# Optimization experiments

Measured on AMD Instinct MI355X. Metric: run time of the kernel, lower is better.

Reference implementation:

```python
import jax, jax.numpy as jnp
import numpy as np

B, S, D, H, F, V, T, L = 64, 1024, 256, 256, 128, 50000, 64, 8
H2 = 2 * H
DIN = H2 + D + 3 * F  # 1152


def setup_inputs() -> dict:
    key = jax.random.key(0)
    ks = jax.random.split(key, 12)
    sd = 0.05
    return {
        "word_ids": jax.random.randint(ks[0], (B, S), 1, V, dtype=jnp.int32),
        "embed": jax.random.normal(ks[1], (V, D), jnp.float32) * sd,
        "encoder_outputs": jax.random.normal(ks[2], (B, S, H2), jnp.float32) * sd,
        "wconv1": jax.random.normal(ks[3], (F, 1, D), jnp.float32) * sd,
        "bconv1": jax.random.normal(ks[4], (F,), jnp.float32) * sd,
        "wconv2": jax.random.normal(ks[5], (F, 2, D), jnp.float32) * sd,
        "bconv2": jax.random.normal(ks[6], (F,), jnp.float32) * sd,
        "wconv3": jax.random.normal(ks[7], (F, 3, D), jnp.float32) * sd,
        "bconv3": jax.random.normal(ks[8], (F,), jnp.float32) * sd,
        "W_ih": jax.random.normal(ks[9], (4 * H2, DIN), jnp.float32) * sd,
        "W_hh": jax.random.normal(ks[10], (4 * H2, H2), jnp.float32) * sd,
        "W_fc": jax.random.normal(ks[11], (T, H2), jnp.float32) * sd,
        "seg_len": L,
    }


def reference(word_ids, embed, encoder_outputs, wconv1, bconv1, wconv2, bconv2,
              wconv3, bconv3, W_ih, W_hh, W_fc, seg_len):
    b, s = word_ids.shape
    d = embed.shape[1]
    h2 = encoder_outputs.shape[-1]
    h = h2 // 2
    nseg = s // seg_len

    # word features via embedding lookup (WordFeature with single 'word' feature)
    wf = embed[word_ids]                                  # [B, S, D]
    xs = wf.reshape(b, nseg, seg_len, d)                  # [B, nseg, L, D]
    c_w = xs.mean(axis=2)                                 # [B, nseg, D]
    es = encoder_outputs.reshape(b, nseg, seg_len, h2)
    c_h = es.mean(axis=2)                                 # [B, nseg, 2H]

    # char-CNN per segment: conv2d(1->F, (fs, D)) == 1D conv over time with D in-channels
    xc = xs.reshape(b * nseg, seg_len, d).transpose(0, 2, 1)  # [N, D, L]

    def conv_pool(w, bias):
        k = w.transpose(0, 2, 1)                          # [F, D, fs]
        y = jax.lax.conv_general_dilated(xc, k, window_strides=(1,),
                                         padding="VALID",
                                         dimension_numbers=("NCH", "OIH", "NCH"))
        y = jax.nn.relu(y + bias[None, :, None])
        return y.max(axis=2)                              # max-pool over time -> [N, F]

    c_x = jnp.concatenate([conv_pool(wconv1, bconv1),
                           conv_pool(wconv2, bconv2),
                           conv_pool(wconv3, bconv3)], axis=1)
    c_x = c_x.reshape(b, nseg, -1)                        # [B, nseg, 3F]

    dec_in = jnp.concatenate([c_w, c_h, c_x], axis=-1)    # [B, nseg, DIN]

    # decoder init: fwd-last / bwd-first encoder states
    h0 = jnp.concatenate([encoder_outputs[:, -1, :h], encoder_outputs[:, 0, h:]], axis=1)
    c0 = jnp.zeros_like(h0)

    def step(carry, x):
        hh, cc = carry
        gates = x @ W_ih.T + hh @ W_hh.T                  # [B, 4*2H]
        i, fg, g, o = jnp.split(gates, 4, axis=1)
        cc = jax.nn.sigmoid(fg) * cc + jax.nn.sigmoid(i) * jnp.tanh(g)
        hh = jax.nn.sigmoid(o) * jnp.tanh(cc)
        out = jax.nn.log_softmax(hh @ W_fc.T, axis=-1)
        return (hh, cc), out

    _, outs = jax.lax.scan(step, (h0, c0), dec_in.transpose(1, 0, 2))  # [nseg, B, T]
    return outs.transpose(1, 0, 2).reshape(b * nseg, -1)  # batch-major like the torch loop
```

## Files before the change

kernel.cpp:

```cpp
#include <hip/hip_runtime.h>
#include <math.h>

#define BB   64
#define SS   1024
#define DD   256
#define H2   512
#define FF   128
#define TT   64
#define NSEG 128
#define DIN  1152
#define G4   2048
#define MROWS 8192
#define MX   65536

typedef __attribute__((ext_vector_type(8))) short bf16x8;
typedef __attribute__((ext_vector_type(4))) float f32x4;

__device__ __forceinline__ unsigned short f2b(float f){
    union { float f; unsigned u; } v; v.f = f;
    unsigned r = v.u + 0x7fffu + ((v.u >> 16) & 1u);
    return (unsigned short)(r >> 16);
}
__device__ __forceinline__ float b2f(unsigned short h){
    union { unsigned u; float f; } v; v.u = ((unsigned)h) << 16;
    return v.f;
}
__device__ __forceinline__ float fsig(float x){
    return 1.f / (1.f + __expf(-x));
}
__device__ __forceinline__ float ftanh(float x){
    float e = __expf(-2.f * fabsf(x));
    float r = (1.f - e) / (1.f + e);
    return x < 0.f ? -r : r;
}


__global__ void k_cvt(const float* __restrict__ src, unsigned short* __restrict__ dst, int n){
    int i = blockIdx.x * 256 + threadIdx.x;
    if (i < n) dst[i] = f2b(src[i]);
}

__global__ void k_wf(const float* __restrict__ w1, const float* __restrict__ w2,
                     const float* __restrict__ w3, unsigned short* __restrict__ Wf){
    int i = blockIdx.x * 256 + threadIdx.x;
    int col = i >> 8, d = i & 255;
    float v;
    if (col < 128)      v = w1[col * 256 + d];
    else if (col < 384) { int f = (col - 128) & 127; int tap = (col - 128) >> 7; v = w2[f * 512 + tap * 256 + d]; }
    else                { int c = col - 384; int f = c & 127; int tap = c >> 7;  v = w3[f * 768 + tap * 256 + d]; }
    Wf[i] = f2b(v);
}

__global__ void k_tr_wfc(const float* __restrict__ src, float* __restrict__ dst){
    int i = blockIdx.x * 256 + threadIdx.x;
    int v = i >> 9, k = i & 511;
    dst[k * 64 + v] = src[i];
}

__global__ void k_gather(const int* __restrict__ wid, const float* __restrict__ embed,
                         unsigned short* __restrict__ X){
    int i = blockIdx.x * 256 + threadIdx.x;
    int row = i >> 6, d4 = i & 63;
    int w = wid[row];
    float4 v = *(const float4*)(embed + (size_t)w * DD + d4 * 4);
    ushort4 o; o.x = f2b(v.x); o.y = f2b(v.y); o.z = f2b(v.z); o.w = f2b(v.w);
    *(ushort4*)(X + (size_t)row * DD + d4 * 4) = o;
}

__global__ void k_cw(const unsigned short* __restrict__ X, unsigned short* __restrict__ dec){
    int i = blockIdx.x * 256 + threadIdx.x;
    int row = i >> 8, d = i & 255;
    const unsigned short* p = X + (size_t)row * 8 * DD + d;
    float s = 0.f;
#pragma unroll
    for (int t = 0; t < 8; t++) s += b2f(p[t * DD]);
    dec[(size_t)row * DIN + d] = f2b(s * 0.125f);
}

__global__ void k_ch(const float* __restrict__ enc, unsigned short* __restrict__ dec){
    int i = blockIdx.x * 256 + threadIdx.x;
    int row = i >> 9, c = i & 511;
    const float* p = enc + (size_t)row * 8 * H2 + c;
    float s = 0.f;
#pragma unroll
    for (int t = 0; t < 8; t++) s += p[t * H2];
    dec[(size_t)row * DIN + 256 + c] = f2b(s * 0.125f);
}

__global__ void k_h0(const float* __restrict__ enc, unsigned short* __restrict__ Hbuf){
    int i = blockIdx.x * 256 + threadIdx.x;
    int b = i >> 9, c = i & 511;
    float v = (c < 256) ? enc[(size_t)b * SS * H2 + (size_t)(SS - 1) * H2 + c]
                        : enc[(size_t)b * SS * H2 + c];
    v = fminf(fmaxf(v, -1.875f), 1.875f);
    Hbuf[(size_t)b * 512 + c] = f2b(v);
}

__global__ void k_fill(uint4* __restrict__ p){
    int i = blockIdx.x * 256 + threadIdx.x;
    uint4 v; v.x = v.y = v.z = v.w = 0x7FC07FC0u;
    p[i] = v;
}

__global__ __launch_bounds__(256) void gemm_bt(
    const unsigned short* __restrict__ A, const unsigned short* __restrict__ Bm,
    unsigned short* __restrict__ C, int M, int N, int K)
{
    __shared__ unsigned short As[128][40];
    __shared__ unsigned short Bs[128][40];
    const int tid = threadIdx.x;
    const int m0 = blockIdx.y * 128, n0 = blockIdx.x * 128;
    const int w = tid >> 6, lane = tid & 63;
    const int lm = lane & 15, quad = lane >> 4;
    const int wm = (w >> 1) * 64, wn = (w & 1) * 64;

    const f32x4 z = {0.f, 0.f, 0.f, 0.f};
    f32x4 acc[4][4];
#pragma unroll
    for (int i = 0; i < 4; i++)
#pragma unroll
        for (int j = 0; j < 4; j++) acc[i][j] = z;

    const int r0 = tid >> 2;
    const int kp = (tid & 3) * 8;

    for (int kc = 0; kc < K; kc += 32){
        uint4 a0 = *(const uint4*)(A + (size_t)(m0 + r0) * K + kc + kp);
        uint4 a1 = *(const uint4*)(A + (size_t)(m0 + 64 + r0) * K + kc + kp);
        uint4 b0 = *(const uint4*)(Bm + (size_t)(n0 + r0) * K + kc + kp);
        uint4 b1 = *(const uint4*)(Bm + (size_t)(n0 + 64 + r0) * K + kc + kp);
        __syncthreads();
        *(uint4*)&As[r0][kp] = a0;
        *(uint4*)&As[64 + r0][kp] = a1;
        *(uint4*)&Bs[r0][kp] = b0;
        *(uint4*)&Bs[64 + r0][kp] = b1;
        __syncthreads();
        bf16x8 af[4], bf[4];
#pragma unroll
        for (int mt = 0; mt < 4; mt++) af[mt] = *(const bf16x8*)&As[wm + mt * 16 + lm][quad * 8];
#pragma unroll
        for (int nt = 0; nt < 4; nt++) bf[nt] = *(const bf16x8*)&Bs[wn + nt * 16 + lm][quad * 8];
#pragma unroll
        for (int mt = 0; mt < 4; mt++)
#pragma unroll
            for (int nt = 0; nt < 4; nt++)
                acc[mt][nt] = __builtin_amdgcn_mfma_f32_16x16x32_bf16(af[mt], bf[nt], acc[mt][nt], 0, 0, 0);
    }
#pragma unroll
    for (int mt = 0; mt < 4; mt++){
        int mrow = m0 + wm + mt * 16 + quad * 4;
#pragma unroll
        for (int nt = 0; nt < 4; nt++){
            int ncol = n0 + wn + nt * 16 + lm;
#pragma unroll
            for (int r = 0; r < 4; r++)
                C[(size_t)(mrow + r) * N + ncol] = f2b(acc[mt][nt][r]);
        }
    }
}

__global__ __launch_bounds__(256) void gemm_bt_gates(
    const unsigned short* __restrict__ A, const unsigned short* __restrict__ Bm,
    unsigned short* __restrict__ C, int M, int N, int K)
{
    __shared__ unsigned short As[128][40];
    __shared__ unsigned short Bs[128][40];
    const int tid = threadIdx.x;
    const int m0 = blockIdx.y * 128, n0 = blockIdx.x * 128;
    const int w = tid >> 6, lane = tid & 63;
    const int lm = lane & 15, quad = lane >> 4;
    const int wm = (w >> 1) * 64, wn = (w & 1) * 64;

    const f32x4 z = {0.f, 0.f, 0.f, 0.f};
    f32x4 acc[4][4];
#pragma unroll
    for (int i = 0; i < 4; i++)
#pragma unroll
        for (int j = 0; j < 4; j++) acc[i][j] = z;

    const int r0 = tid >> 2;
    const int kp = (tid & 3) * 8;

    for (int kc = 0; kc < K; kc += 32){
        uint4 a0 = *(const uint4*)(A + (size_t)(m0 + r0) * K + kc + kp);
        uint4 a1 = *(const uint4*)(A + (size_t)(m0 + 64 + r0) * K + kc + kp);
        uint4 b0 = *(const uint4*)(Bm + (size_t)(n0 + r0) * K + kc + kp);
        uint4 b1 = *(const uint4*)(Bm + (size_t)(n0 + 64 + r0) * K + kc + kp);
        __syncthreads();
        *(uint4*)&As[r0][kp] = a0;
        *(uint4*)&As[64 + r0][kp] = a1;
        *(uint4*)&Bs[r0][kp] = b0;
        *(uint4*)&Bs[64 + r0][kp] = b1;
        __syncthreads();
        bf16x8 af[4], bf[4];
#pragma unroll
        for (int mt = 0; mt < 4; mt++) af[mt] = *(const bf16x8*)&As[wm + mt * 16 + lm][quad * 8];
#pragma unroll
        for (int nt = 0; nt < 4; nt++) bf[nt] = *(const bf16x8*)&Bs[wn + nt * 16 + lm][quad * 8];
#pragma unroll
        for (int mt = 0; mt < 4; mt++)
#pragma unroll
            for (int nt = 0; nt < 4; nt++)
                acc[mt][nt] = __builtin_amdgcn_mfma_f32_16x16x32_bf16(af[mt], bf[nt], acc[mt][nt], 0, 0, 0);
    }
#pragma unroll
    for (int mt = 0; mt < 4; mt++){
        int mrow = m0 + wm + mt * 16 + quad * 4;
#pragma unroll
        for (int nt = 0; nt < 4; nt++){
            int ncol = n0 + wn + nt * 16 + lm;
            int g = ncol >> 9, c = ncol & 511;
            int gb = c >> 5, hcl = c & 31;
            int n = hcl * 4 + g;
#pragma unroll
            for (int r = 0; r < 4; r++){
                int m = mrow + r;
                int b = m >> 7, t = m & 127;
                int grp = b >> 4, bl = b & 15;
                size_t dst = (((size_t)(grp * 16 + gb) * NSEG + t) * 128 + n) * 16 + bl;
                C[dst] = f2b(acc[mt][nt][r]);
            }
        }
    }
}

__global__ void k_pool(const unsigned short* __restrict__ G, const float* __restrict__ bias,
                       unsigned short* __restrict__ dec, int taps, int colofs){
    int i = blockIdx.x * 256 + threadIdx.x;
    int row = i >> 7, f = i & 127;
    int N = taps * 128;
    float mx = -1e30f;
    for (int t = 0; t <= 8 - taps; t++){
        float a = 0.f;
        for (int tap = 0; tap < taps; tap++)
            a += b2f(G[(size_t)(row * 8 + t + tap) * N + tap * 128 + f]);
        mx = fmaxf(mx, a);
    }
    mx = fmaxf(mx + bias[f], 0.f);
    dec[(size_t)row * DIN + 768 + colofs + f] = f2b(mx);
}

__global__ __launch_bounds__(256, 1) void k_lstm(
    const unsigned short* __restrict__ gxt,
    const unsigned short* __restrict__ Whh,
    unsigned short* __restrict__ Hbuf)
{
    __shared__ unsigned short W_lds[128 * 512];
    __shared__ unsigned short h_lds[16 * 512];
    __shared__ unsigned short hpk[4 * 128];

    const int tid = threadIdx.x;
    const int nb = blockIdx.x;
    const int grp = nb >> 4, gb = nb & 15;
    const int w = tid >> 6, lane = tid & 63, lm = lane & 15, quad = lane >> 4;
    const int g = lm & 3;

#pragma unroll
    for (int i = 0; i < 32; i++){
        int c = i * 256 + tid;
        int n = c >> 6, kc = c & 63;
        int grow = (n & 3) * 512 + gb * 32 + (n >> 2);
        uint4 v = *(const uint4*)(Whh + (size_t)grow * H2 + kc * 8);
        unsigned addr = ((unsigned)n << 10) + ((unsigned)kc << 4);
        addr ^= (unsigned)(n & 7) << 4;
        *(uint4*)((char*)W_lds + addr) = v;
    }
    __syncthreads();

    const char* wb = (const char*)W_lds;
    const unsigned r0b = (unsigned)(w * 32 + lm) << 10;
    const unsigned r1b = r0b + (16u << 10);
    const unsigned swz = (unsigned)(lm & 7) << 4;

    float cst[2][4] = {{0.f,0.f,0.f,0.f},{0.f,0.f,0.f,0.f}};

    union Chunk { unsigned long long q[2]; uint4 u4; };

    for (int t = 0; t < NSEG; t++){
        const unsigned short* hsrc = Hbuf + (size_t)t * (BB * H2) + (size_t)grp * (16 * H2);
        Chunk ch[4];
#pragma unroll
        for (int j = 0; j < 4; j++){
            const unsigned long long* p = (const unsigned long long*)(hsrc + (size_t)(j * 256 + tid) * 8);
            ch[j].q[0] = __hip_atomic_load(p,     __ATOMIC_RELAXED, __HIP_MEMORY_SCOPE_AGENT);
            ch[j].q[1] = __hip_atomic_load(p + 1, __ATOMIC_RELAXED, __HIP_MEMORY_SCOPE_AGENT);
        }

        const unsigned short* gchunk = gxt + ((size_t)nb * NSEG + t) * 2048;
        ushort4 pr0 = *(const ushort4*)(gchunk + (w * 32 + lm) * 16 + quad * 4);
        ushort4 pr1 = *(const ushort4*)(gchunk + (w * 32 + 16 + lm) * 16 + quad * 4);

        unsigned pend = 0xFu;
        while (pend){
            unsigned np = 0;
#pragma unroll
            for (int j = 0; j < 4; j++){
                if (pend & (1u << j)){
                    if (((ch[j].q[0] | ch[j].q[1]) & 0x4000400040004000ULL) != 0ULL){
                        const unsigned long long* p = (const unsigned long long*)(hsrc + (size_t)(j * 256 + tid) * 8);
                        ch[j].q[0] = __hip_atomic_load(p,     __ATOMIC_RELAXED, __HIP_MEMORY_SCOPE_AGENT);
                        ch[j].q[1] = __hip_atomic_load(p + 1, __ATOMIC_RELAXED, __HIP_MEMORY_SCOPE_AGENT);
                        np |= 1u << j;
                    }
                }
            }
            pend = np;
            if (pend) __builtin_amdgcn_s_sleep(1);
        }

        char* hb = (char*)h_lds;
#pragma unroll
        for (int j = 0; j < 4; j++){
            unsigned addr = (unsigned)(j * 256 + tid) * 16u;
            addr ^= ((addr >> 10) & 7u) << 4;
            *(uint4*)(hb + addr) = ch[j].u4;
        }
        __syncthreads();

        const unsigned hrowb = (unsigned)lm << 10;
        f32x4 acc0 = {0.f,0.f,0.f,0.f}, acc1 = {0.f,0.f,0.f,0.f};
#pragma unroll
        for (int ks = 0; ks < 16; ks++){
            unsigned colb = ((unsigned)ks << 6) + ((unsigned)quad << 4);
            bf16x8 avv = *(const bf16x8*)(hb + ((hrowb + colb) ^ swz));
            bf16x8 w0  = *(const bf16x8*)(wb + ((r0b  + colb) ^ swz));
            bf16x8 w1  = *(const bf16x8*)(wb + ((r1b  + colb) ^ swz));
            acc0 = __builtin_amdgcn_mfma_f32_16x16x32_bf16(avv, w0, acc0, 0, 0, 0);
            acc1 = __builtin_amdgcn_mfma_f32_16x16x32_bf16(avv, w1, acc1, 0, 0, 0);
        }
        __syncthreads();

        const unsigned short* pr0s = (const unsigned short*)&pr0;
        const unsigned short* pr1s = (const unsigned short*)&pr1;
#pragma unroll
        for (int nt = 0; nt < 2; nt++){
#pragma unroll
            for (int r = 0; r < 4; r++){
                float a = (nt ? acc1[r] : acc0[r]) + b2f(nt ? pr1s[r] : pr0s[r]);
                float bsw = __shfl_xor(a, 1);
                float p  = (g & 1) ? bsw : a;
                float qq = (g & 1) ? a : bsw;
                float c2 = __shfl_xor(p, 2);
                float d2 = __shfl_xor(qq, 2);
                float iv = (g & 2) ? c2 : p;
                float gv = (g & 2) ? p  : c2;
                float fv = (g & 2) ? d2 : qq;
                float ov = (g & 2) ? qq : d2;
                float si = fsig(iv), sf = fsig(fv), so = fsig(ov);
                float cn = sf * cst[nt][r] + si * ftanh(gv);
                cst[nt][r] = cn;
                unsigned short hv = f2b(so * ftanh(cn));
                if (hv & 0x4000u) hv = 0;
                if (g == 0)
                    hpk[w * 128 + (quad * 4 + r) * 8 + nt * 4 + (lm >> 2)] = hv;
            }
        }
        asm volatile("s_waitcnt lgkmcnt(0)" ::: "memory");
        __builtin_amdgcn_sched_barrier(0);
        if (lane < 16){
            const unsigned long long* sp = (const unsigned long long*)&hpk[w * 128 + lane * 8];
            unsigned long long s0 = sp[0], s1 = sp[1];
            unsigned long long* dp = (unsigned long long*)
                (Hbuf + (size_t)(t + 1) * (BB * H2) + (size_t)(grp * 16 + lane) * H2 + gb * 32 + w * 8);
            __hip_atomic_store(dp,     s0, __ATOMIC_RELAXED, __HIP_MEMORY_SCOPE_AGENT);
            __hip_atomic_store(dp + 1, s1, __ATOMIC_RELAXED, __HIP_MEMORY_SCOPE_AGENT);
        }
        asm volatile("" ::: "memory");
    }
}

__global__ __launch_bounds__(256) void k_out(
    const unsigned short* __restrict__ Hbuf, const float* __restrict__ Wt, float* __restrict__ out)
{
    __shared__ float hsh[4][H2];
    const int w = threadIdx.x >> 6, lane = threadIdx.x & 63;
    const int row = blockIdx.x * 4 + w;
    const int b = row >> 7, t = row & 127;
    const unsigned short* hp = Hbuf + (size_t)(t + 1) * (BB * H2) + (size_t)b * H2;
    uint4 hv = *(const uint4*)(hp + lane * 8);
    const unsigned short* hs = (const unsigned short*)&hv;
#pragma unroll
    for (int i = 0; i < 8; i++) hsh[w][lane * 8 + i] = b2f(hs[i]);
    __syncthreads();
    float acc = 0.f;
#pragma unroll 8
    for (int k = 0; k < H2; k++)
        acc = fmaf(hsh[w][k], Wt[k * 64 + lane], acc);
    float m = acc;
#pragma unroll
    for (int off = 32; off; off >>= 1) m = fmaxf(m, __shfl_xor(m, off));
    float e = expf(acc - m), s = e;
#pragma unroll
    for (int off = 32; off; off >>= 1) s += __shfl_xor(s, off);
    out[(size_t)row * TT + lane] = acc - m - logf(s);
}

extern "C" void kernel_launch(void* const* d_in, const int* in_sizes, int n_in,
                              void* d_out, int out_size, void* d_ws, size_t ws_size,
                              hipStream_t stream)
{
    const int*   wid = (const int*)d_in[0];
    const float* emb = (const float*)d_in[1];
    const float* enc = (const float*)d_in[2];
    const float* wc1 = (const float*)d_in[3];
    const float* bc1 = (const float*)d_in[4];
    const float* wc2 = (const float*)d_in[5];
    const float* bc2 = (const float*)d_in[6];
    const float* wc3 = (const float*)d_in[7];
    const float* bc3 = (const float*)d_in[8];
    const float* wih = (const float*)d_in[9];
    const float* whh = (const float*)d_in[10];
    const float* wfc = (const float*)d_in[11];

    char* ws = (char*)d_ws;
    size_t off = 0;
    auto alloc = [&](size_t bytes) -> void* {
        void* p = ws + off; off += (bytes + 255) & ~(size_t)255; return p;
    };
    unsigned short* X    = (unsigned short*)alloc((size_t)MX * DD * 2);
    unsigned short* dec  = (unsigned short*)alloc((size_t)MROWS * DIN * 2);
    unsigned short* Gb   = (unsigned short*)alloc((size_t)MX * 384 * 2);
    unsigned short* Wfb  = (unsigned short*)alloc((size_t)768 * 256 * 2);
    unsigned short* Wihb = (unsigned short*)alloc((size_t)G4 * DIN * 2);
    unsigned short* Whhb = (unsigned short*)alloc((size_t)G4 * H2 * 2);
    float*          Wfct = (float*)alloc((size_t)H2 * TT * 4);
    unsigned short* Hbuf  = X;
    unsigned short* gates = Gb;

    k_cvt<<<(G4 * DIN + 255) / 256, 256, 0, stream>>>(wih, Wihb, G4 * DIN);
    k_cvt<<<(G4 * H2 + 255) / 256, 256, 0, stream>>>(whh, Whhb, G4 * H2);
    k_wf<<<768, 256, 0, stream>>>(wc1, wc2, wc3, Wfb);
    k_tr_wfc<<<128, 256, 0, stream>>>(wfc, Wfct);
    k_gather<<<MX / 4, 256, 0, stream>>>(wid, emb, X);
    k_cw<<<MROWS, 256, 0, stream>>>(X, dec);
    k_ch<<<MROWS * 2, 256, 0, stream>>>(enc, dec);

    gemm_bt<<<dim3(1, 512), 256, 0, stream>>>(X, Wfb,                         Gb, MX, 128, 256);
    k_pool<<<4096, 256, 0, stream>>>(Gb, bc1, dec, 1, 0);
    gemm_bt<<<dim3(2, 512), 256, 0, stream>>>(X, Wfb + (size_t)128 * 256,     Gb, MX, 256, 256);
    k_pool<<<4096, 256, 0, stream>>>(Gb, bc2, dec, 2, 128);
    gemm_bt<<<dim3(3, 512), 256, 0, stream>>>(X, Wfb + (size_t)384 * 256,     Gb, MX, 384, 256);
    k_pool<<<4096, 256, 0, stream>>>(Gb, bc3, dec, 3, 256);

    k_h0<<<BB * H2 / 256, 256, 0, stream>>>(enc, Hbuf);
    k_fill<<<2048, 256, 0, stream>>>((uint4*)(Hbuf + BB * H2));

    gemm_bt_gates<<<dim3(16, 64), 256, 0, stream>>>(dec, Wihb, gates, MROWS, G4, DIN);
    k_lstm<<<64, 256, 0, stream>>>(gates, Whhb, Hbuf);
    k_out<<<2048, 256, 0, stream>>>(Hbuf, Wfct, (float*)d_out);
}
```

Measured before the change: 1.285 ms.

## Keep LSTM recurrent weights in registers with 8 waves and double-buffered h

The persistent LSTM kernel now uses 512 threads per block, so each wave owns one 16-column MFMA tile and holds its slice of W_hh in VGPRs instead of LDS. The h tile in LDS is double-buffered, which drops the second barrier per step, and hidden outputs are packed with lane shuffles rather than staged through an LDS scratch buffer. This targets the serial per-step latency of the recurrence: fewer LDS reads of weights, one fewer sync, and more waves to hide latency. The cost is heavy register pressure from 16 bf16x8 weight fragments held per lane, plus more, smaller atomic stores per step.

After: 1.098 ms. 14.5% less time.

```diff
diff --git a/kernel.cpp b/kernel.cpp
--- a/kernel.cpp
+++ b/kernel.cpp
@@ -240,14 +240,12 @@
     dec[(size_t)row * DIN + 768 + colofs + f] = f2b(mx);
 }
 
-__global__ __launch_bounds__(256, 1) void k_lstm(
+__global__ __launch_bounds__(512, 2) void k_lstm(
     const unsigned short* __restrict__ gxt,
     const unsigned short* __restrict__ Whh,
     unsigned short* __restrict__ Hbuf)
 {
-    __shared__ unsigned short W_lds[128 * 512];
-    __shared__ unsigned short h_lds[16 * 512];
-    __shared__ unsigned short hpk[4 * 128];
+    __shared__ unsigned short h_lds[2][16 * 512];
 
     const int tid = threadIdx.x;
     const int nb = blockIdx.x;
@@ -255,49 +253,42 @@
     const int w = tid >> 6, lane = tid & 63, lm = lane & 15, quad = lane >> 4;
     const int g = lm & 3;
 
-#pragma unroll
-    for (int i = 0; i < 32; i++){
-        int c = i * 256 + tid;
-        int n = c >> 6, kc = c & 63;
-        int grow = (n & 3) * 512 + gb * 32 + (n >> 2);
-        uint4 v = *(const uint4*)(Whh + (size_t)grow * H2 + kc * 8);
-        unsigned addr = ((unsigned)n << 10) + ((unsigned)kc << 4);
-        addr ^= (unsigned)(n & 7) << 4;
-        *(uint4*)((char*)W_lds + addr) = v;
-    }
-    __syncthreads();
-
-    const char* wb = (const char*)W_lds;
-    const unsigned r0b = (unsigned)(w * 32 + lm) << 10;
-    const unsigned r1b = r0b + (16u << 10);
-    const unsigned swz = (unsigned)(lm & 7) << 4;
-
-    float cst[2][4] = {{0.f,0.f,0.f,0.f},{0.f,0.f,0.f,0.f}};
+    bf16x8 wf[16];
+    {
+        int n = w * 16 + lm;
+        const unsigned short* p = Whh + (size_t)((n & 3) * 512 + gb * 32 + (n >> 2)) * H2 + quad * 8;
+#pragma unroll
+        for (int ks = 0; ks < 16; ks++) wf[ks] = *(const bf16x8*)(p + ks * 32);
+    }
+
+    float cst[4] = {0.f, 0.f, 0.f, 0.f};
 
     union Chunk { unsigned long long q[2]; uint4 u4; };
 
     for (int t = 0; t < NSEG; t++){
+#pragma unroll
+        for (int ks = 0; ks < 16; ks++) asm volatile("" : "+v"(wf[ks]));
+
         const unsigned short* hsrc = Hbuf + (size_t)t * (BB * H2) + (size_t)grp * (16 * H2);
-        Chunk ch[4];
-#pragma unroll
-        for (int j = 0; j < 4; j++){
-            const unsigned long long* p = (const unsigned long long*)(hsrc + (size_t)(j * 256 + tid) * 8);
+        Chunk ch[2];
+#pragma unroll
+        for (int j = 0; j < 2; j++){
+            const unsigned long long* p = (const unsigned long long*)(hsrc + (size_t)(j * 512 + tid) * 8);
             ch[j].q[0] = __hip_atomic_load(p,     __ATOMIC_RELAXED, __HIP_MEMORY_SCOPE_AGENT);
             ch[j].q[1] = __hip_atomic_load(p + 1, __ATOMIC_RELAXED, __HIP_MEMORY_SCOPE_AGENT);
         }
 
         const unsigned short* gchunk = gxt + ((size_t)nb * NSEG + t) * 2048;
-        ushort4 pr0 = *(const ushort4*)(gchunk + (w * 32 + lm) * 16 + quad * 4);
-        ushort4 pr1 = *(const ushort4*)(gchunk + (w * 32 + 16 + lm) * 16 + quad * 4);
-
-        unsigned pend = 0xFu;
+        ushort4 pr = *(const ushort4*)(gchunk + (w * 16 + lm) * 16 + quad * 4);
+
+        unsigned pend = 0x3u;
         while (pend){
             unsigned np = 0;
 #pragma unroll
-            for (int j = 0; j < 4; j++){
+            for (int j = 0; j < 2; j++){
                 if (pend & (1u << j)){
                     if (((ch[j].q[0] | ch[j].q[1]) & 0x4000400040004000ULL) != 0ULL){
-                        const unsigned long long* p = (const unsigned long long*)(hsrc + (size_t)(j * 256 + tid) * 8);
+                        const unsigned long long* p = (const unsigned long long*)(hsrc + (size_t)(j * 512 + tid) * 8);
                         ch[j].q[0] = __hip_atomic_load(p,     __ATOMIC_RELAXED, __HIP_MEMORY_SCOPE_AGENT);
                         ch[j].q[1] = __hip_atomic_load(p + 1, __ATOMIC_RELAXED, __HIP_MEMORY_SCOPE_AGENT);
                         np |= 1u << j;
@@ -308,62 +299,58 @@
             if (pend) __builtin_amdgcn_s_sleep(1);
         }
 
-        char* hb = (char*)h_lds;
-#pragma unroll
-        for (int j = 0; j < 4; j++){
-            unsigned addr = (unsigned)(j * 256 + tid) * 16u;
+        char* hb = (char*)&h_lds[t & 1][0];
+#pragma unroll
+        for (int j = 0; j < 2; j++){
+            unsigned addr = (unsigned)(j * 512 + tid) * 16u;
             addr ^= ((addr >> 10) & 7u) << 4;
             *(uint4*)(hb + addr) = ch[j].u4;
         }
         __syncthreads();
 
         const unsigned hrowb = (unsigned)lm << 10;
-        f32x4 acc0 = {0.f,0.f,0.f,0.f}, acc1 = {0.f,0.f,0.f,0.f};
+        const unsigned swz = (unsigned)(lm & 7) << 4;
+        f32x4 acc = {0.f, 0.f, 0.f, 0.f};
 #pragma unroll
         for (int ks = 0; ks < 16; ks++){
             unsigned colb = ((unsigned)ks << 6) + ((unsigned)quad << 4);
             bf16x8 avv = *(const bf16x8*)(hb + ((hrowb + colb) ^ swz));
-            bf16x8 w0  = *(const bf16x8*)(wb + ((r0b  + colb) ^ swz));
-            bf16x8 w1  = *(const bf16x8*)(wb + ((r1b  + colb) ^ swz));
-            acc0 = __builtin_amdgcn_mfma_f32_16x16x32_bf16(avv, w0, acc0, 0, 0, 0);
-            acc1 = __builtin_amdgcn_mfma_f32_16x16x32_bf16(avv, w1, acc1, 0, 0, 0);
-        }
-        __syncthreads();
-
-        const unsigned short* pr0s = (const unsigned short*)&pr0;
-        const unsigned short* pr1s = (const unsigned short*)&pr1;
-#pragma unroll
-        for (int nt = 0; nt < 2; nt++){
-#pragma unroll
-            for (int r = 0; r < 4; r++){
-                float a = (nt ? acc1[r] : acc0[r]) + b2f(nt ? pr1s[r] : pr0s[r]);
-                float bsw = __shfl_xor(a, 1);
-                float p  = (g & 1) ? bsw : a;
-                float qq = (g & 1) ? a : bsw;
-                float c2 = __shfl_xor(p, 2);
-                float d2 = __shfl_xor(qq, 2);
-                float iv = (g & 2) ? c2 : p;
-                float gv = (g & 2) ? p  : c2;
-                float fv = (g & 2) ? d2 : qq;
-                float ov = (g & 2) ? qq : d2;
-                float si = fsig(iv), sf = fsig(fv), so = fsig(ov);
-                float cn = sf * cst[nt][r] + si * ftanh(gv);
-                cst[nt][r] = cn;
-                unsigned short hv = f2b(so * ftanh(cn));
-                if (hv & 0x4000u) hv = 0;
-                if (g == 0)
-                    hpk[w * 128 + (quad * 4 + r) * 8 + nt * 4 + (lm >> 2)] = hv;
+            acc = __builtin_amdgcn_mfma_f32_16x16x32_bf16(avv, wf[ks], acc, 0, 0, 0);
+        }
+
+        const unsigned short* prs = (const unsigned short*)&pr;
+        unsigned short hv4[4];
+#pragma unroll
+        for (int r = 0; r < 4; r++){
+            float a = acc[r] + b2f(prs[r]);
+            float bsw = __shfl_xor(a, 1);
+            float p  = (g & 1) ? bsw : a;
+            float qq = (g & 1) ? a : bsw;
+            float c2 = __shfl_xor(p, 2);
+            float d2 = __shfl_xor(qq, 2);
+            float iv = (g & 2) ? c2 : p;
+            float gv = (g & 2) ? p  : c2;
+            float fv = (g & 2) ? d2 : qq;
+            float ov = (g & 2) ? qq : d2;
+            float si = fsig(iv), sf = fsig(fv), so = fsig(ov);
+            float cn = sf * cst[r] + si * ftanh(gv);
+            cst[r] = cn;
+            unsigned short hv = f2b(so * ftanh(cn));
+            if (hv & 0x4000u) hv = 0;
+            hv4[r] = hv;
+        }
+
+#pragma unroll
+        for (int r = 0; r < 4; r++){
+            unsigned v01 = (unsigned)hv4[r] | ((unsigned)(unsigned short)__shfl_xor((int)hv4[r], 4) << 16);
+            unsigned v23 = (unsigned)__shfl_xor((int)v01, 8);
+            unsigned long long outq = (unsigned long long)v01 | ((unsigned long long)v23 << 32);
+            if (lm == 0){
+                int bt = grp * 16 + quad * 4 + r;
+                unsigned long long* dp = (unsigned long long*)
+                    (Hbuf + (size_t)(t + 1) * (BB * H2) + (size_t)bt * H2 + gb * 32 + w * 4);
+                __hip_atomic_store(dp, outq, __ATOMIC_RELAXED, __HIP_MEMORY_SCOPE_AGENT);
             }
-        }
-        asm volatile("s_waitcnt lgkmcnt(0)" ::: "memory");
-        __builtin_amdgcn_sched_barrier(0);
-        if (lane < 16){
-            const unsigned long long* sp = (const unsigned long long*)&hpk[w * 128 + lane * 8];
-            unsigned long long s0 = sp[0], s1 = sp[1];
-            unsigned long long* dp = (unsigned long long*)
-                (Hbuf + (size_t)(t + 1) * (BB * H2) + (size_t)(grp * 16 + lane) * H2 + gb * 32 + w * 8);
-            __hip_atomic_store(dp,     s0, __ATOMIC_RELAXED, __HIP_MEMORY_SCOPE_AGENT);
-            __hip_atomic_store(dp + 1, s1, __ATOMIC_RELAXED, __HIP_MEMORY_SCOPE_AGENT);
         }
         asm volatile("" ::: "memory");
     }
@@ -446,6 +433,6 @@
     k_fill<<<2048, 256, 0, stream>>>((uint4*)(Hbuf + BB * H2));
 
     gemm_bt_gates<<<dim3(16, 64), 256, 0, stream>>>(dec, Wihb, gates, MROWS, G4, DIN);
-    k_lstm<<<64, 256, 0, stream>>>(gates, Whhb, Hbuf);
+    k_lstm<<<64, 512, 0, stream>>>(gates, Whhb, Hbuf);
     k_out<<<2048, 256, 0, stream>>>(Hbuf, Wfct, (float*)d_out);
 }
```
